# Kernel tuning notes

Measured on AMD Instinct MI355X. Metric: run time of the kernel, lower is better.

## Reference

```python
import jax, jax.numpy as jnp
import numpy as np

B, S, D, H, L, FF, V, TYPES = 16, 512, 1024, 16, 8, 4096, 30522, 2
DH = D // H
BETA = 1.0          # pbit_temperature
EPS = 1e-12         # layer_norm_eps
STD = 0.02          # initializer_range


def _ln(x, g, b):
    m = x.mean(-1, keepdims=True)
    v = ((x - m) ** 2).mean(-1, keepdims=True)
    return (x - m) * jax.lax.rsqrt(v + EPS) * g + b


def setup_inputs() -> dict:
    key = jax.random.key(0)
    ks = iter(jax.random.split(key, 32))
    rn = lambda shape: (jax.random.normal(next(ks), shape, dtype=jnp.float32) * STD)
    inp = {
        'input_ids': jax.random.randint(next(ks), (B, S), 0, V),
        'token_type_ids': jax.random.randint(next(ks), (B, S), 0, TYPES),
        'tok_emb': rn((V, D)),
        'pos_emb': rn((S, D)),
        'type_emb': rn((TYPES, D)),
        'emb_g': jnp.ones((D,), jnp.float32),
        'emb_b': jnp.zeros((D,), jnp.float32),
        # stacked per-layer parameters [L, ...]
        'Wq': rn((L, D, D)), 'bq': jnp.zeros((L, D), jnp.float32),
        'Wk': rn((L, D, D)), 'bk': jnp.zeros((L, D), jnp.float32),
        'Wv': rn((L, D, D)), 'bv': jnp.zeros((L, D), jnp.float32),
        'Wo': rn((L, D, D)), 'bo': jnp.zeros((L, D), jnp.float32),
        'ln1_g': jnp.ones((L, D), jnp.float32), 'ln1_b': jnp.zeros((L, D), jnp.float32),
        'ln2_g': jnp.ones((L, D), jnp.float32), 'ln2_b': jnp.zeros((L, D), jnp.float32),
        'W1': rn((L, D, FF)), 'b1': jnp.zeros((L, FF), jnp.float32),
        'W2': rn((L, FF, D)), 'b2': jnp.zeros((L, D), jnp.float32),
    }
    return inp


def reference(input_ids, token_type_ids, tok_emb, pos_emb, type_emb, emb_g, emb_b,
              Wq, bq, Wk, bk, Wv, bv, Wo, bo, ln1_g, ln1_b, ln2_g, ln2_b,
              W1, b1, W2, b2):
    # Embeddings (eval mode: TSU noise + dropout are identity)
    h = tok_emb[input_ids] + pos_emb[None, :, :] + type_emb[token_type_ids]
    h = _ln(h, emb_g, emb_b)

    def layer(h, p):
        wq, bq_, wk, bk_, wv, bv_, wo, bo_, g1, bb1, g2, bb2, w1, bf1, w2, bf2 = p
        x = _ln(h, g1, bb1)  # pre-LN per TinyBioBERTLayer
        q = (x @ wq + bq_).reshape(B, S, H, DH)
        k = (x @ wk + bk_).reshape(B, S, H, DH)
        v = (x @ wv + bv_).reshape(B, S, H, DH)
        # P-bit attention in expectation == temperature-scaled softmax SDPA
        scores = jnp.einsum('bqhd,bkhd->bhqk', q, k) * (BETA / np.sqrt(DH))
        a = jax.nn.softmax(scores, axis=-1)
        ctx = jnp.einsum('bhqk,bkhd->bqhd', a, v).reshape(B, S, D)
        h = h + ctx @ wo + bo_
        y = _ln(h, g2, bb2)
        y = jax.nn.gelu(y @ w1 + bf1, approximate=False) @ w2 + bf2
        return h + y, None

    params = (Wq, bq, Wk, bk, Wv, bv, Wo, bo, ln1_g, ln1_b, ln2_g, ln2_b, W1, b1, W2, b2)
    h, _ = jax.lax.scan(layer, h, params)
    return h
```

## Files before the change

kernel.cpp:

```cpp
#include <hip/hip_runtime.h>
#include <math.h>

#define B_  16
#define S_  512
#define D_  1024
#define H_  16
#define DH_ 64
#define L_  8
#define FF_ 4096
#define M_  (B_*S_)

typedef __attribute__((ext_vector_type(4))) float  f32x4;
typedef __attribute__((ext_vector_type(8))) short  s8v;
typedef __attribute__((ext_vector_type(4))) short  s4v;
typedef __attribute__((ext_vector_type(8))) __bf16 bf8v;

__device__ __forceinline__ short f2bf(float f) {
  union { float f; unsigned u; } x; x.f = f;
  unsigned r = x.u + 0x7fffu + ((x.u >> 16) & 1u);
  return (short)(r >> 16);
}

__device__ __forceinline__ f32x4 mfma16(s8v a, s8v b, f32x4 c) {
  return __builtin_amdgcn_mfma_f32_16x16x32_bf16(
      __builtin_bit_cast(bf8v, a), __builtin_bit_cast(bf8v, b), c, 0, 0, 0);
}

__device__ __forceinline__ void gl_lds16(const void* g, void* lds) {
  __builtin_amdgcn_global_load_lds(
      (const __attribute__((address_space(1))) unsigned int*)g,
      (__attribute__((address_space(3))) unsigned int*)lds, 16, 0, 0);
}

__device__ __forceinline__ float gelu_f(float v) {
  const float t  = 0.7978845608f * (v + 0.044715f * v * v * v);
  const float e  = __expf(-2.0f * fabsf(t));
  const float th = copysignf((1.f - e) / (1.f + e), t);
  return 0.5f * v * (1.0f + th);
}

__global__ __launch_bounds__(256) void tcvt(const float* __restrict__ src,
                                            short* __restrict__ dst, int R, int C,
                                            size_t dls) {
  __shared__ float tile[32][33];
  src += (size_t)blockIdx.z * R * C;
  dst += (size_t)blockIdx.z * dls;
  const int c0 = blockIdx.x * 32, r0 = blockIdx.y * 32;
  const int tx = threadIdx.x & 31, ty = threadIdx.x >> 5;
#pragma unroll
  for (int i = 0; i < 32; i += 8)
    tile[ty + i][tx] = src[(size_t)(r0 + ty + i) * C + (c0 + tx)];
  __syncthreads();
#pragma unroll
  for (int i = 0; i < 32; i += 8)
    dst[(size_t)(c0 + ty + i) * R + (r0 + tx)] = f2bf(tile[tx][ty + i]);
}

__global__ __launch_bounds__(256) void embed_ln(
    const int* __restrict__ ids, const int* __restrict__ tts,
    const float* __restrict__ tok, const float* __restrict__ pos,
    const float* __restrict__ typ, const float* __restrict__ g,
    const float* __restrict__ bta, float* __restrict__ h) {
  const int row = blockIdx.x;
  const int s = row & (S_ - 1);
  const int id = ids[row], tt = tts[row];
  const int t = threadIdx.x;
  const float4 a = ((const float4*)(tok + (size_t)id * D_))[t];
  const float4 p = ((const float4*)(pos + (size_t)s  * D_))[t];
  const float4 y = ((const float4*)(typ + (size_t)tt * D_))[t];
  float x0 = a.x + p.x + y.x, x1 = a.y + p.y + y.y;
  float x2 = a.z + p.z + y.z, x3 = a.w + p.w + y.w;
  float sum = x0 + x1 + x2 + x3;
  float sq  = x0*x0 + x1*x1 + x2*x2 + x3*x3;
  __shared__ float red[8];
#pragma unroll
  for (int d = 1; d < 64; d <<= 1) { sum += __shfl_xor(sum, d); sq += __shfl_xor(sq, d); }
  if ((t & 63) == 0) { red[t >> 6] = sum; red[(t >> 6) + 4] = sq; }
  __syncthreads();
  sum = red[0] + red[1] + red[2] + red[3];
  sq  = red[4] + red[5] + red[6] + red[7];
  const float mean = sum * (1.f / D_);
  const float var  = sq * (1.f / D_) - mean * mean;
  const float rstd = rsqrtf(fmaxf(var, 0.f) + 1e-12f);
  const float4 gg = ((const float4*)g)[t];
  const float4 bb = ((const float4*)bta)[t];
  float4 o;
  o.x = (x0 - mean) * rstd * gg.x + bb.x;
  o.y = (x1 - mean) * rstd * gg.y + bb.y;
  o.z = (x2 - mean) * rstd * gg.z + bb.z;
  o.w = (x3 - mean) * rstd * gg.w + bb.w;
  ((float4*)(h + (size_t)row * D_))[t] = o;
}

__global__ __launch_bounds__(256) void ln_bf16(
    const float* __restrict__ h, const float* __restrict__ g,
    const float* __restrict__ bta, short* __restrict__ out) {
  const int row = blockIdx.x;
  const int t = threadIdx.x;
  const float4 x = ((const float4*)(h + (size_t)row * D_))[t];
  float sum = x.x + x.y + x.z + x.w;
  float sq  = x.x*x.x + x.y*x.y + x.z*x.z + x.w*x.w;
  __shared__ float red[8];
#pragma unroll
  for (int d = 1; d < 64; d <<= 1) { sum += __shfl_xor(sum, d); sq += __shfl_xor(sq, d); }
  if ((t & 63) == 0) { red[t >> 6] = sum; red[(t >> 6) + 4] = sq; }
  __syncthreads();
  sum = red[0] + red[1] + red[2] + red[3];
  sq  = red[4] + red[5] + red[6] + red[7];
  const float mean = sum * (1.f / D_);
  const float var  = sq * (1.f / D_) - mean * mean;
  const float rstd = rsqrtf(fmaxf(var, 0.f) + 1e-12f);
  const float4 gg = ((const float4*)g)[t];
  const float4 bb = ((const float4*)bta)[t];
  s4v o;
  o[0] = f2bf((x.x - mean) * rstd * gg.x + bb.x);
  o[1] = f2bf((x.y - mean) * rstd * gg.y + bb.y);
  o[2] = f2bf((x.z - mean) * rstd * gg.z + bb.z);
  o[3] = f2bf((x.w - mean) * rstd * gg.w + bb.w);
  *(s4v*)&out[(size_t)row * D_ + t * 4] = o;
}

__global__ __launch_bounds__(256) void ln_red(
    float* __restrict__ h, const float* __restrict__ p0,
    const float* __restrict__ p1, const float* __restrict__ badd,
    const float* __restrict__ g, const float* __restrict__ bta,
    short* __restrict__ out) {
  const int row = blockIdx.x;
  const int t = threadIdx.x;
  const size_t off = (size_t)row * D_;
  float4 x = ((const float4*)(h + off))[t];
  const float4 a = ((const float4*)(p0 + off))[t];
  const float4 b = ((const float4*)(p1 + off))[t];
  const float4 c = ((const float4*)badd)[t];
  x.x += a.x + b.x + c.x; x.y += a.y + b.y + c.y;
  x.z += a.z + b.z + c.z; x.w += a.w + b.w + c.w;
  ((float4*)(h + off))[t] = x;
  float sum = x.x + x.y + x.z + x.w;
  float sq  = x.x*x.x + x.y*x.y + x.z*x.z + x.w*x.w;
  __shared__ float red[8];
#pragma unroll
  for (int d = 1; d < 64; d <<= 1) { sum += __shfl_xor(sum, d); sq += __shfl_xor(sq, d); }
  if ((t & 63) == 0) { red[t >> 6] = sum; red[(t >> 6) + 4] = sq; }
  __syncthreads();
  sum = red[0] + red[1] + red[2] + red[3];
  sq  = red[4] + red[5] + red[6] + red[7];
  const float mean = sum * (1.f / D_);
  const float var  = sq * (1.f / D_) - mean * mean;
  const float rstd = rsqrtf(fmaxf(var, 0.f) + 1e-12f);
  const float4 gg = ((const float4*)g)[t];
  const float4 bb = ((const float4*)bta)[t];
  s4v o;
  o[0] = f2bf((x.x - mean) * rstd * gg.x + bb.x);
  o[1] = f2bf((x.y - mean) * rstd * gg.y + bb.y);
  o[2] = f2bf((x.z - mean) * rstd * gg.z + bb.z);
  o[3] = f2bf((x.w - mean) * rstd * gg.w + bb.w);
  *(s4v*)&out[off + t * 4] = o;
}

__global__ __launch_bounds__(256) void final_add(
    float* __restrict__ h, const float* __restrict__ p0,
    const float* __restrict__ p1, const float* __restrict__ badd) {
  const int row = blockIdx.x;
  const int t = threadIdx.x;
  const size_t off = (size_t)row * D_;
  float4 x = ((const float4*)(h + off))[t];
  const float4 a = ((const float4*)(p0 + off))[t];
  const float4 b = ((const float4*)(p1 + off))[t];
  const float4 c = ((const float4*)badd)[t];
  x.x += a.x + b.x + c.x; x.y += a.y + b.y + c.y;
  x.z += a.z + b.z + c.z; x.w += a.w + b.w + c.w;
  ((float4*)(h + off))[t] = x;
}

template<int MODE>
__global__ __launch_bounds__(512, 1) void gemm8(
    const short* __restrict__ A, const short* __restrict__ Bt,
    const float* __restrict__ b0, const float* __restrict__ b1,
    const float* __restrict__ b2, short* __restrict__ out,
    float* __restrict__ hres, int N, int K, int LD, int nby) {
  __shared__ __align__(16) char lds[131072];
  const int tid = threadIdx.x, wid = tid >> 6, lane = tid & 63;
  const int wr = wid >> 2, wc = wid & 3;
  const int l15 = lane & 15, l4 = lane >> 4;

  const int n8 = (int)gridDim.x >> 3;
  const int bid = (int)blockIdx.x;
  const int xcd = bid & 7, tt_ = bid >> 3;
  const int nbv = (MODE == 4) ? nby * 2 : nby;
  const int cpx = n8 / nbv;
  const int bx = xcd * cpx + tt_ / nbv;
  const int bv = tt_ % nbv;
  const int by = (MODE == 4) ? (bv & 3) : bv;
  const int slice = (MODE == 4) ? (bv >> 2) : 0;

  const short* __restrict__ Ab = A + (size_t)bx * 256 * LD + (size_t)slice * K;
  const short* __restrict__ Bb = Bt + (size_t)by * 256 * LD + (size_t)slice * K;

  const int str0 = tid >> 3;
  const int stc  = (((tid & 7) ^ (str0 & 7)) * 8);
  const int r7  = l15 & 7;
  const int kx0 = ((l4) ^ r7) * 16;
  const int kx1 = ((4 + l4) ^ r7) * 16;
  const int arow = (wr * 128 + l15) * 128;
  const int brow = (wc * 64 + l15) * 128;

  f32x4 acc[8][4];
#pragma unroll
  for (int m = 0; m < 8; ++m)
#pragma unroll
    for (int n = 0; n < 4; ++n) acc[m][n] = f32x4{0.f, 0.f, 0.f, 0.f};
  s8v af[8][2], bf[4][2];

  const int nt = K >> 6, it = nt >> 1;

#define BAR_ __builtin_amdgcn_s_barrier()
#define LGKM0_ asm volatile("s_waitcnt lgkmcnt(0)" ::: "memory")
#define VMC_(n) asm volatile("s_waitcnt vmcnt(" #n ")" ::: "memory")
#define ST_(isB, slot, hh, kt) do { \
    const short* _g = ((isB) ? Bb : Ab) + (size_t)((hh) * 128 + str0) * LD + ((kt) << 6) + stc; \
    char* _d = lds + ((isB) ? 65536 : 0) + (slot) * 32768 + (hh) * 16384 + wid * 1024; \
    gl_lds16(_g, _d); \
    gl_lds16(_g + (size_t)64 * LD, _d + 8192); \
  } while (0)
#define RDA4_(slot, g) do { \
    const char* _p = lds + (slot) * 32768 + arow + (g) * 8192; \
    _Pragma("unroll") for (int _i = 0; _i < 4; ++_i) { \
      af[(g)*4+_i][0] = *(const s8v*)(_p + _i * 2048 + kx0); \
      af[(g)*4+_i][1] = *(const s8v*)(_p + _i * 2048 + kx1); } \
  } while (0)
#define RDB2_(slot, g) do { \
    const char* _p = lds + 65536 + (slot) * 32768 + brow + (g) * 4096; \
    _Pragma("unroll") for (int _i = 0; _i < 2; ++_i) { \
      bf[(g)*2+_i][0] = *(const s8v*)(_p + _i * 2048 + kx0); \
      bf[(g)*2+_i][1] = *(const s8v*)(_p + _i * 2048 + kx1); } \
  } while (0)
#define MM_(mq, nq) do { \
    __builtin_amdgcn_s_setprio(1); \
    _Pragma("unroll") for (int _mf = 0; _mf < 4; ++_mf) \
    _Pragma("unroll") for (int _nf = 0; _nf < 2; ++_nf) \
    _Pragma("unroll") for (int _ks = 0; _ks < 2; ++_ks) \
      acc[(mq)*4+_mf][(nq)*2+_nf] = \
        mfma16(bf[(nq)*2+_nf][_ks], af[(mq)*4+_mf][_ks], acc[(mq)*4+_mf][(nq)*2+_nf]); \
    __builtin_amdgcn_s_setprio(0); \
  } while (0)

  ST_(1,0,0,0); ST_(1,0,1,0); ST_(0,0,0,0); ST_(0,0,1,0);
  ST_(1,1,0,1); ST_(0,1,0,1); ST_(0,1,1,1);
  VMC_(6);
  BAR_;

  for (int t = 0; t < it; ++t) {
    const int ka = 2 * t, kb = ka + 1;
    const bool s2 = (ka + 2) < nt, s3 = (kb + 2) < nt;
    RDA4_(0, 0); RDB2_(0, 0);
    ST_(1, 1, 1, kb);
    BAR_; LGKM0_; MM_(0, 0); BAR_;
    RDB2_(0, 1);
    BAR_; LGKM0_; MM_(0, 1); BAR_;
    RDA4_(0, 1);
    if (s2) ST_(1, 0, 0, ka + 2);
    BAR_; LGKM0_; MM_(1, 0); BAR_;
    if (s2) { ST_(1, 0, 1, ka + 2); VMC_(4); } else { VMC_(0); }
    BAR_; MM_(1, 1); BAR_;
    RDA4_(1, 0); RDB2_(1, 0);
    if (s2) ST_(0, 0, 0, ka + 2);
    BAR_; LGKM0_; MM_(0, 0); BAR_;
    RDB2_(1, 1);
    if (s2) ST_(0, 0, 1, ka + 2);
    BAR_; LGKM0_; MM_(0, 1); BAR_;
    RDA4_(1, 1);
    if (s3) ST_(1, 1, 0, kb + 2);
    BAR_; LGKM0_; MM_(1, 0); BAR_;
    if (s3) { ST_(0, 1, 0, kb + 2); ST_(0, 1, 1, kb + 2); VMC_(6); }
    BAR_; MM_(1, 1); BAR_;
  }

  const int r0 = bx * 256 + wr * 128;
  const int c0 = by * 256 + wc * 64;
  const int which = (MODE == 3) ? (c0 >> 10) : 0;
  const float* __restrict__ bias =
      (MODE == 3) ? (which == 0 ? b0 : (which == 1 ? b1 : b2)) : b0;
  short* __restrict__ outw = (MODE == 3) ? out + (size_t)which * M_ * D_ : out;
  float* __restrict__ pp =
      (MODE == 4) ? hres + (size_t)slice * ((size_t)M_ * D_) : hres;
#pragma unroll
  for (int n = 0; n < 4; ++n) {
    const int colb = c0 + n * 16 + l4 * 4;
    const int colw = colb & (D_ - 1);
    float4 bb4 = {0.f, 0.f, 0.f, 0.f};
    if (MODE == 3)                       bb4 = *(const float4*)&bias[colw];
    else if (MODE != 4 && bias)          bb4 = *(const float4*)&bias[colb];
#pragma unroll
    for (int m = 0; m < 8; ++m) {
      const int row = r0 + m * 16 + l15;
      float v0 = acc[m][n][0] + bb4.x, v1 = acc[m][n][1] + bb4.y;
      float v2 = acc[m][n][2] + bb4.z, v3 = acc[m][n][3] + bb4.w;
      if (MODE == 2) {
        float4* hp = (float4*)&hres[(size_t)row * N + colb];
        float4 hv = *hp;
        hv.x += v0; hv.y += v1; hv.z += v2; hv.w += v3;
        *hp = hv;
      } else if (MODE == 4) {
        float4 pv; pv.x = v0; pv.y = v1; pv.z = v2; pv.w = v3;
        *(float4*)&pp[(size_t)row * N + colb] = pv;
      } else {
        if (MODE == 1) { v0 = gelu_f(v0); v1 = gelu_f(v1); v2 = gelu_f(v2); v3 = gelu_f(v3); }
        s4v pk;
        pk[0] = f2bf(v0); pk[1] = f2bf(v1); pk[2] = f2bf(v2); pk[3] = f2bf(v3);
        if (MODE == 3) {
          const int b = row >> 9, s = row & 511, hd = colw >> 6, dh = colw & 63;
          *(s4v*)&outw[((((size_t)b * H_ + hd) * S_ + s) << 6) + dh] = pk;
        } else {
          *(s4v*)&outw[(size_t)row * N + colb] = pk;
        }
      }
    }
  }
#undef BAR_
#undef LGKM0_
#undef VMC_
#undef ST_
#undef RDA4_
#undef RDB2_
#undef MM_
}

__global__ __launch_bounds__(256, 2) void attn(
    const short* __restrict__ Q, const short* __restrict__ K,
    const short* __restrict__ V, short* __restrict__ ctx) {
  __shared__ __align__(16) short Kl[32][72];
  __shared__ __align__(16) short Vt[DH_][40];
  __shared__ __align__(16) short Pl[4][32 * 40];

  const int tid = threadIdx.x, wid = tid >> 6, lane = tid & 63;
  const int l15 = lane & 15, l4 = lane >> 4;
  const int bh = blockIdx.y;
  const size_t base = (size_t)bh * S_ * DH_;
  const short* Qb = Q + base;
  const short* Kb = K + base;
  const short* Vb = V + base;

  const int qoff = blockIdx.x * 128 + wid * 32;

  s8v qf[2][2];
#pragma unroll
  for (int mf = 0; mf < 2; ++mf)
#pragma unroll
    for (int ks = 0; ks < 2; ++ks)
      qf[mf][ks] = *(const s8v*)&Qb[(size_t)(qoff + mf * 16 + l15) * DH_ + ks * 32 + l4 * 8];

  const f32x4 zero4 = {0.f, 0.f, 0.f, 0.f};
  f32x4 o[2][4];
  float rm[2][4], rs[2][4];
#pragma unroll
  for (int mf = 0; mf < 2; ++mf) {
#pragma unroll
    for (int nf = 0; nf < 4; ++nf) o[mf][nf] = zero4;
#pragma unroll
    for (int r = 0; r < 4; ++r) { rm[mf][r] = -1e30f; rs[mf][r] = 0.f; }
  }

  const int str = tid >> 3;
  const int stc = (tid & 7) * 8;

  for (int kt = 0; kt < S_ / 32; ++kt) {
    __syncthreads();
    {
      const s8v kk = *(const s8v*)&Kb[(size_t)(kt * 32 + str) * DH_ + stc];
      *(s8v*)&Kl[str][stc] = kk;
      const s8v vv = *(const s8v*)&Vb[(size_t)(kt * 32 + str) * DH_ + stc];
#pragma unroll
      for (int j = 0; j < 8; ++j) Vt[stc + j][str] = vv[j];
    }
    __syncthreads();

    f32x4 sc[2][2];
#pragma unroll
    for (int mf = 0; mf < 2; ++mf)
#pragma unroll
      for (int nt = 0; nt < 2; ++nt) sc[mf][nt] = zero4;
#pragma unroll
    for (int nt = 0; nt < 2; ++nt)
#pragma unroll
      for (int ks = 0; ks < 2; ++ks) {
        const s8v kf = *(const s8v*)&Kl[nt * 16 + l15][ks * 32 + l4 * 8];
#pragma unroll
        for (int mf = 0; mf < 2; ++mf)
          sc[mf][nt] = mfma16(qf[mf][ks], kf, sc[mf][nt]);
      }

#pragma unroll
    for (int mf = 0; mf < 2; ++mf) {
      float tm[4];
#pragma unroll
      for (int r = 0; r < 4; ++r) {
        sc[mf][0][r] *= 0.125f; sc[mf][1][r] *= 0.125f;
        tm[r] = fmaxf(sc[mf][0][r], sc[mf][1][r]);
      }
#pragma unroll
      for (int d = 1; d < 16; d <<= 1)
#pragma unroll
        for (int r = 0; r < 4; ++r) tm[r] = fmaxf(tm[r], __shfl_xor(tm[r], d));
      float ps[4];
#pragma unroll
      for (int r = 0; r < 4; ++r) {
        const float nm = fmaxf(rm[mf][r], tm[r]);
        const float so = __expf(rm[mf][r] - nm);
        rm[mf][r] = nm;
        rs[mf][r] *= so;
#pragma unroll
        for (int nf = 0; nf < 4; ++nf) o[mf][nf][r] *= so;
        const float p0 = __expf(sc[mf][0][r] - nm);
        const float p1 = __expf(sc[mf][1][r] - nm);
        sc[mf][0][r] = p0; sc[mf][1][r] = p1;
        ps[r] = p0 + p1;
      }
#pragma unroll
      for (int d = 1; d < 16; d <<= 1)
#pragma unroll
        for (int r = 0; r < 4; ++r) ps[r] += __shfl_xor(ps[r], d);
#pragma unroll
      for (int r = 0; r < 4; ++r) rs[mf][r] += ps[r];
#pragma unroll
      for (int nt = 0; nt < 2; ++nt)
#pragma unroll
        for (int r = 0; r < 4; ++r)
          Pl[wid][(mf * 16 + l4 * 4 + r) * 40 + nt * 16 + l15] = f2bf(sc[mf][nt][r]);
    }
    asm volatile("s_waitcnt lgkmcnt(0)" ::: "memory");

    s8v vf[4];
#pragma unroll
    for (int nf = 0; nf < 4; ++nf)
      vf[nf] = *(const s8v*)&Vt[nf * 16 + l15][l4 * 8];
#pragma unroll
    for (int mf = 0; mf < 2; ++mf) {
      const s8v pf = *(const s8v*)&Pl[wid][(mf * 16 + l15) * 40 + l4 * 8];
#pragma unroll
      for (int nf = 0; nf < 4; ++nf)
        o[mf][nf] = mfma16(pf, vf[nf], o[mf][nf]);
    }
  }

  const int bb = bh >> 4, hh = bh & 15;
#pragma unroll
  for (int mf = 0; mf < 2; ++mf)
#pragma unroll
    for (int r = 0; r < 4; ++r) {
      const int qrow = qoff + mf * 16 + l4 * 4 + r;
      const float inv = 1.0f / rs[mf][r];
      short* dst = ctx + (size_t)(bb * S_ + qrow) * D_ + hh * DH_;
#pragma unroll
      for (int nf = 0; nf < 4; ++nf)
        dst[nf * 16 + l15] = f2bf(o[mf][nf][r] * inv);
    }
}

extern "C" void kernel_launch(void* const* d_in, const int* in_sizes, int n_in,
                              void* d_out, int out_size, void* d_ws, size_t ws_size,
                              hipStream_t stream) {
  const int*   ids = (const int*)d_in[0];
  const int*   tts = (const int*)d_in[1];
  const float* tok = (const float*)d_in[2];
  const float* pos = (const float*)d_in[3];
  const float* typ = (const float*)d_in[4];
  const float* eg  = (const float*)d_in[5];
  const float* eb  = (const float*)d_in[6];
  const float* Wq  = (const float*)d_in[7];  const float* bq = (const float*)d_in[8];
  const float* Wk  = (const float*)d_in[9];  const float* bk = (const float*)d_in[10];
  const float* Wv  = (const float*)d_in[11]; const float* bv = (const float*)d_in[12];
  const float* Wo  = (const float*)d_in[13]; const float* bo = (const float*)d_in[14];
  const float* g1  = (const float*)d_in[15]; const float* be1 = (const float*)d_in[16];
  const float* g2  = (const float*)d_in[17]; const float* be2 = (const float*)d_in[18];
  const float* W1  = (const float*)d_in[19]; const float* b1 = (const float*)d_in[20];
  const float* W2  = (const float*)d_in[21]; const float* b2 = (const float*)d_in[22];

  float* h = (float*)d_out;

  const size_t szDD  = (size_t)D_ * D_;
  const size_t szDF  = (size_t)D_ * FF_;
  const size_t xb_b  = (size_t)M_ * D_ * 2;
  const size_t big_b = (size_t)M_ * FF_ * 2;
  const size_t pa_b  = (size_t)M_ * D_ * 4;
  const size_t wfull = (szDD * 4 + szDF * 2) * 2 * L_;
  const bool full = ws_size >= wfull + xb_b + big_b + 8192;
  const bool sk   = ws_size >= wfull + xb_b + big_b + 2 * pa_b + 8192;

  char* p = (char*)d_ws;
  auto alloc = [&](size_t bytes) { char* r = p; p += (bytes + 255) & ~(size_t)255; return r; };
  const size_t wl = full ? L_ : 1;
  short* wqkvT = (short*)alloc(szDD * 3 * 2 * wl);
  short* woT   = (short*)alloc(szDD * 2 * wl);
  short* w1T   = (short*)alloc(szDF * 2 * wl);
  short* w2T   = (short*)alloc(szDF * 2 * wl);
  short* xb  = (short*)alloc(xb_b);
  char*  big = alloc(big_b);
  float* pa0 = sk ? (float*)alloc(pa_b) : nullptr;
  float* pa1 = sk ? (float*)alloc(pa_b) : nullptr;
  short* qb  = (short*)big;
  short* cb  = xb;
  short* tb  = (short*)big;

  if (full) {
    tcvt<<<dim3(D_/32,  D_/32,  L_), 256, 0, stream>>>(Wq, wqkvT,          D_,  D_,  3*szDD);
    tcvt<<<dim3(D_/32,  D_/32,  L_), 256, 0, stream>>>(Wk, wqkvT +   szDD, D_,  D_,  3*szDD);
    tcvt<<<dim3(D_/32,  D_/32,  L_), 256, 0, stream>>>(Wv, wqkvT + 2*szDD, D_,  D_,  3*szDD);
    tcvt<<<dim3(D_/32,  D_/32,  L_), 256, 0, stream>>>(Wo, woT, D_,  D_,  szDD);
    tcvt<<<dim3(FF_/32, D_/32,  L_), 256, 0, stream>>>(W1, w1T, D_,  FF_, szDF);
    tcvt<<<dim3(D_/32,  FF_/32, L_), 256, 0, stream>>>(W2, w2T, FF_, D_,  szDF);
  }

  embed_ln<<<M_, 256, 0, stream>>>(ids, tts, tok, pos, typ, eg, eb, h);

  const int nbx = M_ / 256;
  for (int l = 0; l < L_; ++l) {
    if (!full) {
      tcvt<<<dim3(D_/32,  D_/32,  1), 256, 0, stream>>>(Wq + (size_t)l*szDD, wqkvT,          D_,  D_,  0);
      tcvt<<<dim3(D_/32,  D_/32,  1), 256, 0, stream>>>(Wk + (size_t)l*szDD, wqkvT +   szDD, D_,  D_,  0);
      tcvt<<<dim3(D_/32,  D_/32,  1), 256, 0, stream>>>(Wv + (size_t)l*szDD, wqkvT + 2*szDD, D_,  D_,  0);
      tcvt<<<dim3(D_/32,  D_/32,  1), 256, 0, stream>>>(Wo + (size_t)l*szDD, woT, D_,  D_,  0);
      tcvt<<<dim3(FF_/32, D_/32,  1), 256, 0, stream>>>(W1 + (size_t)l*szDF, w1T, D_,  FF_, 0);
      tcvt<<<dim3(D_/32,  FF_/32, 1), 256, 0, stream>>>(W2 + (size_t)l*szDF, w2T, FF_, D_,  0);
    }
    const size_t o3 = full ? (size_t)l * 3 * szDD : 0;
    const size_t od = full ? (size_t)l * szDD : 0;
    const size_t of = full ? (size_t)l * szDF : 0;

    if (l == 0 || !sk)
      ln_bf16<<<M_, 256, 0, stream>>>(h, g1 + l*D_, be1 + l*D_, xb);
    else
      ln_red<<<M_, 256, 0, stream>>>(h, pa0, pa1, b2 + (l-1)*D_,
                                     g1 + l*D_, be1 + l*D_, xb);

    gemm8<3><<<nbx * (3*D_/256), 512, 0, stream>>>(
        xb, wqkvT + o3, bq + l*D_, bk + l*D_, bv + l*D_, qb, nullptr, 3*D_, D_, D_, 3*D_/256);
    attn<<<dim3(S_/128, B_*H_), 256, 0, stream>>>(
        qb, qb + (size_t)M_*D_, qb + 2*(size_t)M_*D_, cb);

    if (sk) {
      gemm8<4><<<nbx * (D_/256) * 2, 512, 0, stream>>>(
          cb, woT + od, nullptr, nullptr, nullptr, nullptr, pa0, D_, D_/2, D_, D_/256);
      ln_red<<<M_, 256, 0, stream>>>(h, pa0, pa1, bo + l*D_,
                                     g2 + l*D_, be2 + l*D_, xb);
    } else {
      gemm8<2><<<nbx * (D_/256), 512, 0, stream>>>(
          cb, woT + od, bo + l*D_, nullptr, nullptr, nullptr, h, D_, D_, D_, D_/256);
      ln_bf16<<<M_, 256, 0, stream>>>(h, g2 + l*D_, be2 + l*D_, xb);
    }

    gemm8<1><<<nbx * (FF_/256), 512, 0, stream>>>(
        xb, w1T + of, b1 + l*FF_, nullptr, nullptr, tb, nullptr, FF_, D_, D_, FF_/256);

    if (sk) {
      gemm8<4><<<nbx * (D_/256) * 2, 512, 0, stream>>>(
          tb, w2T + of, nullptr, nullptr, nullptr, nullptr, pa0, D_, FF_/2, FF_, D_/256);
    } else {
      gemm8<2><<<nbx * (D_/256), 512, 0, stream>>>(
          tb, w2T + of, b2 + l*D_, nullptr, nullptr, nullptr, h, D_, FF_, FF_, D_/256);
    }
  }
  if (sk)
    final_add<<<M_, 256, 0, stream>>>(h, pa0, pa1, b2 + (L_-1)*D_);
}
```

Before: 3.188 ms.

## Emit V transposed from projection GEMM and widen attention key tiles

The QKV projection is split in two launches. The V part goes to a new GEMM mode that swaps the MFMA operands and writes V already transposed per head as [b,h,dh,s], so attention no longer does a scalar LDS transpose. The attention kernel now processes 64-key tiles with register prefetch of the next K/V tile, padded LDS strides, MFMA priority hints and a higher occupancy bound. The cost is an extra kernel launch and a strided transposed store in the V GEMM epilogue, and the higher launch bound may add register pressure.

```diff
diff --git a/kernel.cpp b/kernel.cpp
--- a/kernel.cpp
+++ b/kernel.cpp
@@ -238,9 +238,14 @@
     __builtin_amdgcn_s_setprio(1); \
     _Pragma("unroll") for (int _mf = 0; _mf < 4; ++_mf) \
     _Pragma("unroll") for (int _nf = 0; _nf < 2; ++_nf) \
-    _Pragma("unroll") for (int _ks = 0; _ks < 2; ++_ks) \
-      acc[(mq)*4+_mf][(nq)*2+_nf] = \
-        mfma16(bf[(nq)*2+_nf][_ks], af[(mq)*4+_mf][_ks], acc[(mq)*4+_mf][(nq)*2+_nf]); \
+    _Pragma("unroll") for (int _ks = 0; _ks < 2; ++_ks) { \
+      if (MODE == 5) \
+        acc[(mq)*4+_mf][(nq)*2+_nf] = \
+          mfma16(af[(mq)*4+_mf][_ks], bf[(nq)*2+_nf][_ks], acc[(mq)*4+_mf][(nq)*2+_nf]); \
+      else \
+        acc[(mq)*4+_mf][(nq)*2+_nf] = \
+          mfma16(bf[(nq)*2+_nf][_ks], af[(mq)*4+_mf][_ks], acc[(mq)*4+_mf][(nq)*2+_nf]); \
+    } \
     __builtin_amdgcn_s_setprio(0); \
   } while (0)
 
@@ -277,9 +282,27 @@
 
   const int r0 = bx * 256 + wr * 128;
   const int c0 = by * 256 + wc * 64;
+  if (MODE == 5) {
+#pragma unroll
+    for (int n = 0; n < 4; ++n) {
+      const int col = c0 + n * 16 + l15;
+      const int hd = col >> 6, dh = col & 63;
+      const float bb = b0[col];
+#pragma unroll
+      for (int m = 0; m < 8; ++m) {
+        const int row = r0 + m * 16 + l4 * 4;
+        const int b = row >> 9, s = row & 511;
+        s4v pk;
+#pragma unroll
+        for (int rr = 0; rr < 4; ++rr) pk[rr] = f2bf(acc[m][n][rr] + bb);
+        *(s4v*)&out[(((size_t)(b * H_ + hd) * DH_) + dh) * S_ + s] = pk;
+      }
+    }
+    return;
+  }
   const int which = (MODE == 3) ? (c0 >> 10) : 0;
   const float* __restrict__ bias =
-      (MODE == 3) ? (which == 0 ? b0 : (which == 1 ? b1 : b2)) : b0;
+      (MODE == 3) ? (which == 0 ? b0 : b1) : b0;
   short* __restrict__ outw = (MODE == 3) ? out + (size_t)which * M_ * D_ : out;
   float* __restrict__ pp =
       (MODE == 4) ? hres + (size_t)slice * ((size_t)M_ * D_) : hres;
@@ -288,8 +311,8 @@
     const int colb = c0 + n * 16 + l4 * 4;
     const int colw = colb & (D_ - 1);
     float4 bb4 = {0.f, 0.f, 0.f, 0.f};
-    if (MODE == 3)                       bb4 = *(const float4*)&bias[colw];
-    else if (MODE != 4 && bias)          bb4 = *(const float4*)&bias[colb];
+    if (MODE == 3)              bb4 = *(const float4*)&bias[colw];
+    else if (MODE != 4 && bias) bb4 = *(const float4*)&bias[colb];
 #pragma unroll
     for (int m = 0; m < 8; ++m) {
       const int row = r0 + m * 16 + l15;
@@ -325,20 +348,19 @@
 #undef MM_
 }
 
-__global__ __launch_bounds__(256, 2) void attn(
+__global__ __launch_bounds__(256, 4) void attn(
     const short* __restrict__ Q, const short* __restrict__ K,
-    const short* __restrict__ V, short* __restrict__ ctx) {
-  __shared__ __align__(16) short Kl[32][72];
-  __shared__ __align__(16) short Vt[DH_][40];
-  __shared__ __align__(16) short Pl[4][32 * 40];
+    const short* __restrict__ Vt, short* __restrict__ ctx) {
+  __shared__ __align__(16) short Kl[64 * 72];
+  __shared__ __align__(16) short Vl[64 * 72];
+  __shared__ __align__(16) short Pl[4][32 * 72];
 
   const int tid = threadIdx.x, wid = tid >> 6, lane = tid & 63;
   const int l15 = lane & 15, l4 = lane >> 4;
   const int bh = blockIdx.y;
-  const size_t base = (size_t)bh * S_ * DH_;
-  const short* Qb = Q + base;
-  const short* Kb = K + base;
-  const short* Vb = V + base;
+  const short* Qb = Q  + (size_t)bh * S_ * DH_;
+  const short* Kb = K  + (size_t)bh * S_ * DH_;
+  const short* Vb = Vt + (size_t)bh * DH_ * S_;
 
   const int qoff = blockIdx.x * 128 + wid * 32;
 
@@ -349,45 +371,58 @@
     for (int ks = 0; ks < 2; ++ks)
       qf[mf][ks] = *(const s8v*)&Qb[(size_t)(qoff + mf * 16 + l15) * DH_ + ks * 32 + l4 * 8];
 
-  const f32x4 zero4 = {0.f, 0.f, 0.f, 0.f};
   f32x4 o[2][4];
   float rm[2][4], rs[2][4];
 #pragma unroll
   for (int mf = 0; mf < 2; ++mf) {
 #pragma unroll
-    for (int nf = 0; nf < 4; ++nf) o[mf][nf] = zero4;
+    for (int nf = 0; nf < 4; ++nf) o[mf][nf] = f32x4{0.f, 0.f, 0.f, 0.f};
 #pragma unroll
     for (int r = 0; r < 4; ++r) { rm[mf][r] = -1e30f; rs[mf][r] = 0.f; }
   }
 
-  const int str = tid >> 3;
-  const int stc = (tid & 7) * 8;
-
-  for (int kt = 0; kt < S_ / 32; ++kt) {
+  const int srow = tid >> 3;
+  const int sch  = (tid & 7) * 8;
+
+  s8v rk[2], rv[2];
+#pragma unroll
+  for (int r = 0; r < 2; ++r) {
+    rk[r] = *(const s8v*)&Kb[(size_t)(srow + r * 32) * DH_ + sch];
+    rv[r] = *(const s8v*)&Vb[(size_t)(srow + r * 32) * S_ + sch];
+  }
+
+  for (int kt = 0; kt < S_ / 64; ++kt) {
     __syncthreads();
-    {
-      const s8v kk = *(const s8v*)&Kb[(size_t)(kt * 32 + str) * DH_ + stc];
-      *(s8v*)&Kl[str][stc] = kk;
-      const s8v vv = *(const s8v*)&Vb[(size_t)(kt * 32 + str) * DH_ + stc];
-#pragma unroll
-      for (int j = 0; j < 8; ++j) Vt[stc + j][str] = vv[j];
+#pragma unroll
+    for (int r = 0; r < 2; ++r) {
+      *(s8v*)&Kl[(srow + r * 32) * 72 + sch] = rk[r];
+      *(s8v*)&Vl[(srow + r * 32) * 72 + sch] = rv[r];
     }
     __syncthreads();
-
-    f32x4 sc[2][2];
+    if (kt + 1 < S_ / 64) {
+#pragma unroll
+      for (int r = 0; r < 2; ++r) {
+        rk[r] = *(const s8v*)&Kb[(size_t)((kt + 1) * 64 + srow + r * 32) * DH_ + sch];
+        rv[r] = *(const s8v*)&Vb[(size_t)(srow + r * 32) * S_ + (kt + 1) * 64 + sch];
+      }
+    }
+
+    f32x4 sc[2][4];
 #pragma unroll
     for (int mf = 0; mf < 2; ++mf)
 #pragma unroll
-      for (int nt = 0; nt < 2; ++nt) sc[mf][nt] = zero4;
-#pragma unroll
-    for (int nt = 0; nt < 2; ++nt)
+      for (int nt = 0; nt < 4; ++nt) sc[mf][nt] = f32x4{0.f, 0.f, 0.f, 0.f};
+    __builtin_amdgcn_s_setprio(1);
+#pragma unroll
+    for (int nt = 0; nt < 4; ++nt)
 #pragma unroll
       for (int ks = 0; ks < 2; ++ks) {
-        const s8v kf = *(const s8v*)&Kl[nt * 16 + l15][ks * 32 + l4 * 8];
+        const s8v kf = *(const s8v*)&Kl[(nt * 16 + l15) * 72 + ks * 32 + l4 * 8];
 #pragma unroll
         for (int mf = 0; mf < 2; ++mf)
           sc[mf][nt] = mfma16(qf[mf][ks], kf, sc[mf][nt]);
       }
+    __builtin_amdgcn_s_setprio(0);
 
 #pragma unroll
     for (int mf = 0; mf < 2; ++mf) {
@@ -395,7 +430,9 @@
 #pragma unroll
       for (int r = 0; r < 4; ++r) {
         sc[mf][0][r] *= 0.125f; sc[mf][1][r] *= 0.125f;
-        tm[r] = fmaxf(sc[mf][0][r], sc[mf][1][r]);
+        sc[mf][2][r] *= 0.125f; sc[mf][3][r] *= 0.125f;
+        tm[r] = fmaxf(fmaxf(sc[mf][0][r], sc[mf][1][r]),
+                      fmaxf(sc[mf][2][r], sc[mf][3][r]));
       }
 #pragma unroll
       for (int d = 1; d < 16; d <<= 1)
@@ -410,10 +447,14 @@
         rs[mf][r] *= so;
 #pragma unroll
         for (int nf = 0; nf < 4; ++nf) o[mf][nf][r] *= so;
-        const float p0 = __expf(sc[mf][0][r] - nm);
-        const float p1 = __expf(sc[mf][1][r] - nm);
-        sc[mf][0][r] = p0; sc[mf][1][r] = p1;
-        ps[r] = p0 + p1;
+        float psum = 0.f;
+#pragma unroll
+        for (int nt = 0; nt < 4; ++nt) {
+          const float pv = __expf(sc[mf][nt][r] - nm);
+          sc[mf][nt][r] = pv;
+          psum += pv;
+        }
+        ps[r] = psum;
       }
 #pragma unroll
       for (int d = 1; d < 16; d <<= 1)
@@ -422,24 +463,30 @@
 #pragma unroll
       for (int r = 0; r < 4; ++r) rs[mf][r] += ps[r];
 #pragma unroll
-      for (int nt = 0; nt < 2; ++nt)
+      for (int nt = 0; nt < 4; ++nt)
 #pragma unroll
         for (int r = 0; r < 4; ++r)
-          Pl[wid][(mf * 16 + l4 * 4 + r) * 40 + nt * 16 + l15] = f2bf(sc[mf][nt][r]);
+          Pl[wid][(mf * 16 + l4 * 4 + r) * 72 + nt * 16 + l15] = f2bf(sc[mf][nt][r]);
     }
     asm volatile("s_waitcnt lgkmcnt(0)" ::: "memory");
 
-    s8v vf[4];
-#pragma unroll
-    for (int nf = 0; nf < 4; ++nf)
-      vf[nf] = *(const s8v*)&Vt[nf * 16 + l15][l4 * 8];
-#pragma unroll
-    for (int mf = 0; mf < 2; ++mf) {
-      const s8v pf = *(const s8v*)&Pl[wid][(mf * 16 + l15) * 40 + l4 * 8];
+    __builtin_amdgcn_s_setprio(1);
+#pragma unroll
+    for (int ks = 0; ks < 2; ++ks) {
+      s8v pf[2], vf[4];
+#pragma unroll
+      for (int mf = 0; mf < 2; ++mf)
+        pf[mf] = *(const s8v*)&Pl[wid][(mf * 16 + l15) * 72 + ks * 32 + l4 * 8];
 #pragma unroll
       for (int nf = 0; nf < 4; ++nf)
-        o[mf][nf] = mfma16(pf, vf[nf], o[mf][nf]);
-    }
+        vf[nf] = *(const s8v*)&Vl[(nf * 16 + l15) * 72 + ks * 32 + l4 * 8];
+#pragma unroll
+      for (int mf = 0; mf < 2; ++mf)
+#pragma unroll
+        for (int nf = 0; nf < 4; ++nf)
+          o[mf][nf] = mfma16(pf[mf], vf[nf], o[mf][nf]);
+    }
+    __builtin_amdgcn_s_setprio(0);
   }
 
   const int bb = bh >> 4, hh = bh & 15;
@@ -498,6 +545,7 @@
   float* pa0 = sk ? (float*)alloc(pa_b) : nullptr;
   float* pa1 = sk ? (float*)alloc(pa_b) : nullptr;
   short* qb  = (short*)big;
+  short* vb  = (short*)(big + 2 * xb_b);
   short* cb  = xb;
   short* tb  = (short*)big;
 
@@ -532,10 +580,13 @@
       ln_red<<<M_, 256, 0, stream>>>(h, pa0, pa1, b2 + (l-1)*D_,
                                      g1 + l*D_, be1 + l*D_, xb);
 
-    gemm8<3><<<nbx * (3*D_/256), 512, 0, stream>>>(
-        xb, wqkvT + o3, bq + l*D_, bk + l*D_, bv + l*D_, qb, nullptr, 3*D_, D_, D_, 3*D_/256);
+    gemm8<3><<<nbx * (2*D_/256), 512, 0, stream>>>(
+        xb, wqkvT + o3, bq + l*D_, bk + l*D_, nullptr, qb, nullptr, 2*D_, D_, D_, 2*D_/256);
+    gemm8<5><<<nbx * (D_/256), 512, 0, stream>>>(
+        xb, wqkvT + o3 + 2*szDD, bv + l*D_, nullptr, nullptr, vb, nullptr, D_, D_, D_, D_/256);
+
     attn<<<dim3(S_/128, B_*H_), 256, 0, stream>>>(
-        qb, qb + (size_t)M_*D_, qb + 2*(size_t)M_*D_, cb);
+        qb, qb + (size_t)M_*D_, vb, cb);
 
     if (sk) {
       gemm8<4><<<nbx * (D_/256) * 2, 512, 0, stream>>>(
```

Measured after the change: 3.134 ms. About the same (-1.7%).
